# Kernel tuning notes

Hardware: AMD Instinct MI355X
Metric: run time of the kernel (lower is better)

The kernel has to match this reference:

```python
import jax, jax.numpy as jnp
import numpy as np

DIM = 180
HEADS = 6
WH, WW = 8, 8
MLP_HIDDEN = 720
EPS = 1e-5


def _rel_pos_index(wh, ww):
    ch = np.arange(wh)
    cw = np.arange(ww)
    coords = np.stack(np.meshgrid(ch, cw, indexing='ij'))  # [2, wh, ww]
    cf = coords.reshape(2, -1)                              # [2, N]
    rc = cf[:, :, None] - cf[:, None, :]                    # [2, N, N]
    rc = rc.transpose(1, 2, 0).astype(np.int64)             # [N, N, 2]
    rc[..., 0] += wh - 1
    rc[..., 1] += ww - 1
    rc[..., 0] *= 2 * ww - 1
    return rc.sum(-1)                                       # [N, N]


REL_IDX = jnp.asarray(_rel_pos_index(WH, WW))


def setup_inputs() -> dict:
    key = jax.random.key(0)
    ks = jax.random.split(key, 16)
    B, H, W = 8, 128, 128
    C = DIM
    s = lambda k, shape, sc=0.02: jax.random.normal(k, shape, jnp.float32) * sc
    return {
        'x': jax.random.normal(ks[0], (B, H * W, C), jnp.float32),
        'norm1_w': jnp.ones((C,), jnp.float32),
        'norm1_b': jnp.zeros((C,), jnp.float32),
        'qkv_w': s(ks[1], (C, 3 * C)),
        'qkv_b': jnp.zeros((3 * C,), jnp.float32),
        'rel_bias_table': s(ks[2], ((2 * WH - 1) * (2 * WW - 1), HEADS)),
        'proj_w': s(ks[3], (C, C)),
        'proj_b': jnp.zeros((C,), jnp.float32),
        'norm2_w': jnp.ones((C,), jnp.float32),
        'norm2_b': jnp.zeros((C,), jnp.float32),
        'fc1_w': s(ks[4], (C, MLP_HIDDEN)),
        'fc1_b': jnp.zeros((MLP_HIDDEN,), jnp.float32),
        'fc2_w': s(ks[5], (MLP_HIDDEN, C)),
        'fc2_b': jnp.zeros((C,), jnp.float32),
        'H': H,
        'W': W,
    }


def _layernorm(x, w, b):
    mu = jnp.mean(x, axis=-1, keepdims=True)
    var = jnp.var(x, axis=-1, keepdims=True)
    return (x - mu) * jax.lax.rsqrt(var + EPS) * w + b


def _swin_block(x, H, W, p):
    B, N, C = x.shape
    hd = C // HEADS
    scale = hd ** -0.5

    x1 = _layernorm(x, p['norm1_w'], p['norm1_b'])
    x1 = x1.reshape(B, H, W, C)
    # window partition -> [nW, WH*WW, C]
    x1 = x1.reshape(B, H // WH, WH, W // WW, WW, C).transpose(0, 1, 3, 2, 4, 5)
    nW = B * (H // WH) * (W // WW)
    Nw = WH * WW
    xw = x1.reshape(nW, Nw, C)

    qkv = xw @ p['qkv_w'] + p['qkv_b']                      # [nW, Nw, 3C]
    qkv = qkv.reshape(nW, Nw, 3, HEADS, hd).transpose(2, 0, 3, 1, 4)
    q, k, v = qkv[0], qkv[1], qkv[2]                        # [nW, H, Nw, hd]

    bias = p['rel_bias_table'][REL_IDX.reshape(-1)].reshape(Nw, Nw, HEADS)
    bias = bias.transpose(2, 0, 1)                          # [H, Nw, Nw]

    attn = jnp.einsum('whqd,whkd->whqk', q * scale, k) + bias[None]
    attn = jax.nn.softmax(attn, axis=-1)
    o = jnp.einsum('whqk,whkd->whqd', attn, v)              # [nW, H, Nw, hd]
    o = o.transpose(0, 2, 1, 3).reshape(nW, Nw, C)
    o = o @ p['proj_w'] + p['proj_b']

    # window reverse -> [B, H, W, C]
    o = o.reshape(B, H // WH, W // WW, WH, WW, C).transpose(0, 1, 3, 2, 4, 5)
    o = o.reshape(B, N, C)

    x1 = o + x
    x2 = _layernorm(x1, p['norm2_w'], p['norm2_b'])
    x2 = jax.nn.gelu(x2 @ p['fc1_w'] + p['fc1_b'], approximate=False) @ p['fc2_w'] + p['fc2_b']
    return x2 + x1


def reference(x, norm1_w, norm1_b, qkv_w, qkv_b, rel_bias_table, proj_w, proj_b,
              norm2_w, norm2_b, fc1_w, fc1_b, fc2_w, fc2_b, H, W):
    p = dict(norm1_w=norm1_w, norm1_b=norm1_b, qkv_w=qkv_w, qkv_b=qkv_b,
             rel_bias_table=rel_bias_table, proj_w=proj_w, proj_b=proj_b,
             norm2_w=norm2_w, norm2_b=norm2_b, fc1_w=fc1_w, fc1_b=fc1_b,
             fc2_w=fc2_w, fc2_b=fc2_b)
    return _swin_block(x, H, W, p)
```

## Files before the change

kernel.cpp:

```cpp
#include <hip/hip_runtime.h>
#include <hip/hip_bf16.h>

typedef __hip_bfloat16 bf16;
typedef __attribute__((ext_vector_type(8))) short short8;
typedef __attribute__((ext_vector_type(4))) short short4v;
typedef __attribute__((ext_vector_type(4))) float f32x4;

#define C_DIM 180
#define CPAD  192
#define NHEAD 6
#define HD    30
#define HID   720
#define HPAD  768
#define QKVW  576
#define LN_EPS 1e-5f
#define IMG_TOK 16384
#define QSCALE 0.18257418583505536f

static __device__ __forceinline__ bf16 f2bf(float f) { return __float2bfloat16(f); }
static __device__ __forceinline__ float bf2f(bf16 v) { return __bfloat162float(v); }
static __device__ __forceinline__ short bfbits(float f) {
    bf16 b = __float2bfloat16(f); return *reinterpret_cast<short*>(&b);
}
static __device__ __forceinline__ float gelu_tanh(float v) {
    float u = 0.7978845608f * (v + 0.044715f * v * v * v);
    float e = __expf(2.f * u);
    return 0.5f * v * (2.f - 2.f / (e + 1.f));
}

__global__ __launch_bounds__(256) void prep_w(const float* __restrict__ w, bf16* __restrict__ bt,
                                              int K, int N, int Kpad, int Npad) {
    int idx = blockIdx.x * 256 + threadIdx.x;
    if (idx >= Kpad * Npad) return;
    int k = idx % Kpad, n = idx / Kpad;
    float v = (k < K && n < N) ? w[(long)k * N + n] : 0.f;
    bt[idx] = f2bf(v);
}

__global__ __launch_bounds__(256) void prep_wqkv(const float* __restrict__ w, bf16* __restrict__ bt) {
    int idx = blockIdx.x * 256 + threadIdx.x;
    if (idx >= QKVW * CPAD) return;
    int k = idx % CPAD, c = idx / CPAD;
    int mat = c / 192, rem = c % 192;
    int hh = rem >> 5, dd = rem & 31;
    float v = 0.f;
    if (dd < HD && k < C_DIM) {
        v = w[(long)k * 540 + mat * 180 + hh * 30 + dd];
        if (mat == 0) v *= QSCALE;
    }
    bt[idx] = f2bf(v);
}
__global__ __launch_bounds__(256) void prep_bqkv(const float* __restrict__ b, float* __restrict__ bp) {
    int c = blockIdx.x * 256 + threadIdx.x;
    if (c >= QKVW) return;
    int mat = c / 192, rem = c % 192;
    int hh = rem >> 5, dd = rem & 31;
    float v = 0.f;
    if (dd < HD) {
        v = b[mat * 180 + hh * 30 + dd];
        if (mat == 0) v *= QSCALE;
    }
    bp[c] = v;
}

__global__ __launch_bounds__(256) void prep_f1b(const float* __restrict__ b, float* __restrict__ bp) {
    int i = blockIdx.x * 256 + threadIdx.x;
    if (i < HPAD) bp[i] = (i < HID) ? b[i] : 0.f;
}

__global__ __launch_bounds__(256) void prep_bias(const float* __restrict__ tbl,
                                                 float* __restrict__ bias_frag) {
    int idx = blockIdx.x * 256 + threadIdx.x;
    if (idx >= 6144) return;
    int lane = idx & 63;
    int fj = (idx >> 6) & 3;
    int fi = (idx >> 8) & 3;
    int h  = idx >> 10;
    int g = lane >> 4, l15 = lane & 15;
    int kk = fj * 16 + l15;
    int rk = kk >> 3, ck = kk & 7;
    #pragma unroll
    for (int r = 0; r < 4; ++r) {
        int q = fi * 16 + g * 4 + r;
        int rq = q >> 3, cq = q & 7;
        int bidx = (rq - rk + 7) * 15 + (cq - ck + 7);
        bias_frag[idx * 4 + r] = tbl[bidx * NHEAD + h];
    }
}

__global__ __launch_bounds__(256) void ln_kernel(const float* __restrict__ x,
                                                 const float* __restrict__ w,
                                                 const float* __restrict__ b,
                                                 bf16* __restrict__ out, int M) {
    int wave = threadIdx.x >> 6;
    int lane = threadIdx.x & 63;
    long row = (long)blockIdx.x * 4 + wave;
    if (row >= M) return;
    const float* xr = x + row * C_DIM;
    float e0 = xr[lane];
    float e1 = xr[lane + 64];
    float e2 = (lane < C_DIM - 128) ? xr[lane + 128] : 0.f;
    float s  = e0 + e1 + e2;
    float ss = e0*e0 + e1*e1 + e2*e2;
    #pragma unroll
    for (int off = 32; off > 0; off >>= 1) {
        s  += __shfl_xor(s,  off);
        ss += __shfl_xor(ss, off);
    }
    float mean = s * (1.f / C_DIM);
    float var  = ss * (1.f / C_DIM) - mean * mean;
    float rs   = rsqrtf(var + LN_EPS);
    bf16* orow = out + row * CPAD;
    orow[lane]      = f2bf((e0 - mean) * rs * w[lane]      + b[lane]);
    orow[lane + 64] = f2bf((e1 - mean) * rs * w[lane + 64] + b[lane + 64]);
    if (lane < C_DIM - 128)
        orow[lane + 128] = f2bf((e2 - mean) * rs * w[lane + 128] + b[lane + 128]);
    if (lane < CPAD - C_DIM)
        orow[C_DIM + lane] = f2bf(0.f);
}

#define GLL16(gp, lp) \
    __builtin_amdgcn_global_load_lds((const __attribute__((address_space(1))) unsigned int*)(gp), \
                                     (__attribute__((address_space(3))) unsigned int*)(lp), 16, 0, 0)

template<int DO_GELU, int OUT_MODE>
__global__ __launch_bounds__(256) void mfma_gemm(
    const bf16* __restrict__ A, int lda,
    const bf16* __restrict__ Bt,
    const float* __restrict__ bias,
    const float* __restrict__ resid, int nres,
    void* __restrict__ out, int ldo, int nstore,
    int Kpad, int P)
{
    __shared__ __align__(16) short smem[128 * 64 + 64 * 64];
    short* As = smem;
    short* Bs = smem + 128 * 64;
    int tid  = threadIdx.x;
    int lane = tid & 63;
    int wave = tid >> 6;
    int wm = wave >> 1, wn = wave & 1;
    int g4 = lane >> 4, l15 = lane & 15;

    int flat = blockIdx.x;
    int grp  = flat / (8 * P);
    int rem  = flat - grp * 8 * P;
    int p    = rem >> 3;
    long m0  = (long)(grp * 8 + (rem & 7)) * 128;
    int  n0  = p * 64;

    f32x4 acc[4][2] = {};

    int nkt = Kpad >> 6;
    for (int kt = 0; kt < nkt; ++kt) {
        int k0 = kt << 6;
        #pragma unroll
        for (int i = 0; i < 4; ++i) {
            int f = i * 256 + tid;
            int r = f >> 3, c = f & 7;
            const bf16* gp = A + (m0 + r) * (long)lda + k0 + ((c ^ (r & 7)) << 3);
            GLL16(gp, &As[(i * 256 + (wave << 6)) * 8]);
        }
        #pragma unroll
        for (int i = 0; i < 2; ++i) {
            int f = i * 256 + tid;
            int r = f >> 3, c = f & 7;
            const bf16* gp = Bt + (n0 + r) * (long)Kpad + k0 + ((c ^ (r & 7)) << 3);
            GLL16(gp, &Bs[(i * 256 + (wave << 6)) * 8]);
        }
        __syncthreads();
        #pragma unroll
        for (int ks = 0; ks < 2; ++ks) {
            short8 af[4], bfr[2];
            #pragma unroll
            for (int fi = 0; fi < 4; ++fi) {
                int r  = wm * 64 + fi * 16 + l15;
                int ch = ks * 4 + g4;
                af[fi] = *(const short8*)&As[r * 64 + ((ch ^ (r & 7)) << 3)];
            }
            #pragma unroll
            for (int fj = 0; fj < 2; ++fj) {
                int r  = wn * 32 + fj * 16 + l15;
                int ch = ks * 4 + g4;
                bfr[fj] = *(const short8*)&Bs[r * 64 + ((ch ^ (r & 7)) << 3)];
            }
            #pragma unroll
            for (int fi = 0; fi < 4; ++fi)
                #pragma unroll
                for (int fj = 0; fj < 2; ++fj)
                    acc[fi][fj] = __builtin_amdgcn_mfma_f32_16x16x32_bf16(af[fi], bfr[fj], acc[fi][fj], 0, 0, 0);
        }
        __syncthreads();
    }

    if (OUT_MODE == 0) {
        short* Cs = smem;
        #pragma unroll
        for (int fi = 0; fi < 4; ++fi)
            #pragma unroll
            for (int fj = 0; fj < 2; ++fj) {
                int col = wn * 32 + fj * 16 + l15;
                float bv = (n0 + col < nstore) ? bias[n0 + col] : 0.f;
                #pragma unroll
                for (int rg = 0; rg < 4; ++rg) {
                    int row = wm * 64 + fi * 16 + g4 * 4 + rg;
                    float v = acc[fi][fj][rg] + bv;
                    if (DO_GELU) v = gelu_tanh(v);
                    Cs[row * 72 + col] = bfbits(v);
                }
            }
        __syncthreads();
        #pragma unroll
        for (int i = 0; i < 4; ++i) {
            int t = i * 256 + tid;
            int row = t >> 3, c8 = t & 7;
            short8 v = *(const short8*)&Cs[row * 72 + c8 * 8];
            *(short8*)((bf16*)out + (m0 + row) * (long)ldo + n0 + c8 * 8) = v;
        }
    } else {
        float* Cf = (float*)smem;
        int ncols = nstore - n0; if (ncols > 64) ncols = 64;
        int cpr = ncols >> 2;
        #pragma unroll
        for (int hh = 0; hh < 2; ++hh) {
            if (wm == hh) {
                #pragma unroll
                for (int fi = 0; fi < 4; ++fi)
                    #pragma unroll
                    for (int fj = 0; fj < 2; ++fj) {
                        int col = wn * 32 + fj * 16 + l15;
                        float bv = (n0 + col < nstore) ? bias[n0 + col] : 0.f;
                        #pragma unroll
                        for (int rg = 0; rg < 4; ++rg) {
                            int lrow = fi * 16 + g4 * 4 + rg;
                            Cf[lrow * 68 + col] = acc[fi][fj][rg] + bv;
                        }
                    }
            }
            __syncthreads();
            for (int t = tid; t < 64 * cpr; t += 256) {
                int row = t / cpr, cc = (t - row * cpr) * 4;
                long grow = m0 + hh * 64 + row;
                f32x4 v = *(const f32x4*)&Cf[row * 68 + cc];
                if (resid) {
                    f32x4 rv = *(const f32x4*)(resid + grow * (long)nres + n0 + cc);
                    v += rv;
                }
                *(f32x4*)((float*)out + grow * (long)ldo + n0 + cc) = v;
            }
            __syncthreads();
        }
    }
}

__global__ __launch_bounds__(384, 3) void attn_mfma(
    const bf16* __restrict__ qkv,
    const float* __restrict__ bias_frag,
    bf16* __restrict__ o)
{
    __shared__ __align__(16) short lds[6 * 4096];
    int tid  = threadIdx.x;
    int wave = tid >> 6;
    int lane = tid & 63;
    int h = wave;
    int w = blockIdx.x;
    int b = w >> 8, rem = w & 255;
    int wi = rem >> 4, wj = rem & 15;
    long base = (long)b * IMG_TOK + wi * 8 * 128 + wj * 8;
    int g = lane >> 4, l15 = lane & 15;

    short* Vt = &lds[wave * 4096];
    short* Ph = &lds[wave * 4096 + 2048];

    short8 qf[4], kf[4];
    #pragma unroll
    for (int fi = 0; fi < 4; ++fi) {
        int q = fi * 16 + l15;
        long t = base + (q >> 3) * 128 + (q & 7);
        const bf16* rowp = qkv + t * QKVW + h * 32 + g * 8;
        qf[fi] = *(const short8*)(rowp);
        kf[fi] = *(const short8*)(rowp + 192);
    }

    {
        int t = lane;
        const bf16* vp = qkv + (base + (t >> 3) * 128 + (t & 7)) * QKVW + 384 + h * 32;
        short8 v0 = *(const short8*)(vp);
        short8 v1 = *(const short8*)(vp + 8);
        short8 v2 = *(const short8*)(vp + 16);
        short8 v3 = *(const short8*)(vp + 24);
        int ct = t >> 3, t7 = t & 7;
        #pragma unroll
        for (int d = 0; d < 8; ++d)  Vt[d * 64 + ((ct ^ d) << 3) + t7] = v0[d];
        #pragma unroll
        for (int d = 8; d < 16; ++d) Vt[d * 64 + ((ct ^ (d & 7)) << 3) + t7] = v1[d - 8];
        #pragma unroll
        for (int d = 16; d < 24; ++d) Vt[d * 64 + ((ct ^ (d & 7)) << 3) + t7] = v2[d - 16];
        #pragma unroll
        for (int d = 24; d < 32; ++d) Vt[d * 64 + ((ct ^ (d & 7)) << 3) + t7] = v3[d - 24];
    }

    f32x4 S[4][4];
    #pragma unroll
    for (int fi = 0; fi < 4; ++fi)
        #pragma unroll
        for (int fj = 0; fj < 4; ++fj)
            S[fi][fj] = *(const f32x4*)(bias_frag + (((h * 4 + fi) * 4 + fj) * 64 + lane) * 4);
    #pragma unroll
    for (int fi = 0; fi < 4; ++fi)
        #pragma unroll
        for (int fj = 0; fj < 4; ++fj)
            S[fi][fj] = __builtin_amdgcn_mfma_f32_16x16x32_bf16(qf[fi], kf[fj], S[fi][fj], 0, 0, 0);

    f32x4 mrow[4], lsum[4];
    #pragma unroll
    for (int fi = 0; fi < 4; ++fi) {
        f32x4 a = S[fi][0], c = S[fi][2];
        #pragma unroll
        for (int cc = 0; cc < 4; ++cc) {
            a[cc] = fmaxf(a[cc], S[fi][1][cc]);
            c[cc] = fmaxf(c[cc], S[fi][3][cc]);
            a[cc] = fmaxf(a[cc], c[cc]);
        }
        mrow[fi] = a;
    }
    #pragma unroll
    for (int mask = 1; mask <= 8; mask <<= 1)
        #pragma unroll
        for (int fi = 0; fi < 4; ++fi)
            #pragma unroll
            for (int cc = 0; cc < 4; ++cc)
                mrow[fi][cc] = fmaxf(mrow[fi][cc], __shfl_xor(mrow[fi][cc], mask));
    #pragma unroll
    for (int fi = 0; fi < 4; ++fi)
        #pragma unroll
        for (int fj = 0; fj < 4; ++fj)
            #pragma unroll
            for (int cc = 0; cc < 4; ++cc)
                S[fi][fj][cc] = __expf(S[fi][fj][cc] - mrow[fi][cc]);
    #pragma unroll
    for (int fi = 0; fi < 4; ++fi) {
        f32x4 a = S[fi][0] + S[fi][1];
        f32x4 c = S[fi][2] + S[fi][3];
        lsum[fi] = a + c;
    }
    #pragma unroll
    for (int mask = 1; mask <= 8; mask <<= 1)
        #pragma unroll
        for (int fi = 0; fi < 4; ++fi)
            #pragma unroll
            for (int cc = 0; cc < 4; ++cc)
                lsum[fi][cc] += __shfl_xor(lsum[fi][cc], mask);

    f32x4 O[4][2] = {};
    #pragma unroll
    for (int ks = 0; ks < 2; ++ks) {
        #pragma unroll
        for (int fi = 0; fi < 4; ++fi)
            #pragma unroll
            for (int f2 = 0; f2 < 2; ++f2) {
                int fj = ks * 2 + f2;
                int kh = f2 * 16 + l15;
                #pragma unroll
                for (int r = 0; r < 4; ++r) {
                    int q = fi * 16 + g * 4 + r;
                    int c = (kh >> 3) ^ r ^ g;
                    Ph[q * 32 + (c << 3) + (kh & 7)] = bfbits(S[fi][fj][r]);
                }
            }
        short8 vf[2];
        #pragma unroll
        for (int f2 = 0; f2 < 2; ++f2) {
            int d = f2 * 16 + l15;
            int cv = (ks * 4 + g) ^ (d & 7);
            vf[f2] = *(const short8*)&Vt[d * 64 + (cv << 3)];
        }
        #pragma unroll
        for (int fi = 0; fi < 4; ++fi) {
            int q = fi * 16 + l15;
            int cr = g ^ (q & 3) ^ ((q >> 2) & 3);
            short8 pf = *(const short8*)&Ph[q * 32 + (cr << 3)];
            #pragma unroll
            for (int f2 = 0; f2 < 2; ++f2)
                O[fi][f2] = __builtin_amdgcn_mfma_f32_16x16x32_bf16(pf, vf[f2], O[fi][f2], 0, 0, 0);
        }
    }

    #pragma unroll
    for (int fi = 0; fi < 4; ++fi) {
        f32x4 inv;
        #pragma unroll
        for (int cc = 0; cc < 4; ++cc) inv[cc] = 1.f / lsum[fi][cc];
        #pragma unroll
        for (int r = 0; r < 4; ++r) {
            int q = fi * 16 + g * 4 + r;
            long t = base + (q >> 3) * 128 + (q & 7);
            bf16* op = o + t * CPAD + h * HD;
            op[l15] = f2bf(O[fi][0][r] * inv[r]);
            if (l15 < HD - 16)
                op[16 + l15] = f2bf(O[fi][1][r] * inv[r]);
        }
    }
    if (h == 0) {
        long t = base + (lane >> 3) * 128 + (lane & 7);
        bf16* op = o + t * CPAD + C_DIM;
        short4v z4 = {0, 0, 0, 0};
        short8  z8 = {0, 0, 0, 0, 0, 0, 0, 0};
        *(short4v*)(op) = z4;
        *(short8*)(op + 4) = z8;
    }
}

extern "C" void kernel_launch(void* const* d_in, const int* in_sizes, int n_in,
                              void* d_out, int out_size, void* d_ws, size_t ws_size,
                              hipStream_t stream) {
    const float* x    = (const float*)d_in[0];
    const float* n1w  = (const float*)d_in[1];
    const float* n1b  = (const float*)d_in[2];
    const float* qkvw = (const float*)d_in[3];
    const float* qkvb = (const float*)d_in[4];
    const float* tbl  = (const float*)d_in[5];
    const float* pw   = (const float*)d_in[6];
    const float* pb   = (const float*)d_in[7];
    const float* n2w  = (const float*)d_in[8];
    const float* n2b  = (const float*)d_in[9];
    const float* f1w  = (const float*)d_in[10];
    const float* f1b  = (const float*)d_in[11];
    const float* f2w  = (const float*)d_in[12];
    const float* f2b  = (const float*)d_in[13];

    auto al = [](size_t b) { return (b + 255) & ~(size_t)255; };
    char* base = (char*)d_ws;
    size_t off = 0;
    auto alloc = [&](size_t bytes) -> char* { char* p = base + off; off += al(bytes); return p; };

    bf16* wqp  = (bf16*)alloc((size_t)QKVW * CPAD * 2);
    bf16* wp   = (bf16*)alloc((size_t)192 * 192 * 2);
    bf16* wf1  = (bf16*)alloc((size_t)768 * 192 * 2);
    bf16* wf2  = (bf16*)alloc((size_t)192 * 768 * 2);
    float* bfr = (float*)alloc((size_t)6144 * 4 * 4);
    float* f1bp = (float*)alloc((size_t)HPAD * 4);
    float* qbp  = (float*)alloc((size_t)QKVW * 4);
    size_t woff = off;

    size_t r1_per = al((size_t)IMG_TOK * HPAD * 2);
    size_t r2_per = al((size_t)IMG_TOK * CPAD * 2);
    size_t r3_per = al((size_t)IMG_TOK * C_DIM * 4);
    size_t per_img = r1_per + r2_per + r3_per;
    int g = 8;
    while (g > 1 && woff + per_img * (size_t)g > ws_size) g >>= 1;
    int nchunks = 8 / g;
    long Mc = (long)IMG_TOK * g;
    int nm = (int)(Mc / 128);

    bf16*  R1 = (bf16*)(base + woff);
    bf16*  R2 = (bf16*)(base + woff + r1_per * g);
    float* R3 = (float*)(base + woff + (r1_per + r2_per) * g);

    prep_wqkv<<<(QKVW * CPAD + 255) / 256, 256, 0, stream>>>(qkvw, wqp);
    prep_bqkv<<<(QKVW + 255) / 256, 256, 0, stream>>>(qkvb, qbp);
    prep_w<<<(192 * 192 + 255) / 256, 256, 0, stream>>>(pw, wp, 180, 180, 192, 192);
    prep_w<<<(768 * 192 + 255) / 256, 256, 0, stream>>>(f1w, wf1, 180, 720, 192, 768);
    prep_w<<<(192 * 768 + 255) / 256, 256, 0, stream>>>(f2w, wf2, 720, 180, 768, 192);
    prep_bias<<<(6144 + 255) / 256, 256, 0, stream>>>(tbl, bfr);
    prep_f1b<<<(HPAD + 255) / 256, 256, 0, stream>>>(f1b, f1bp);

    for (int ci = 0; ci < nchunks; ++ci) {
        const float* xc   = x + (size_t)ci * Mc * C_DIM;
        float*       outc = (float*)d_out + (size_t)ci * Mc * C_DIM;

        ln_kernel<<<Mc / 4, 256, 0, stream>>>(xc, n1w, n1b, R2, (int)Mc);
        mfma_gemm<0, 0><<<dim3(nm * 9), 256, 0, stream>>>(
            R2, CPAD, wqp, qbp, nullptr, 0, R1, QKVW, QKVW, CPAD, 9);
        attn_mfma<<<dim3(256 * g), 384, 0, stream>>>(R1, bfr, R2);
        mfma_gemm<0, 1><<<dim3(nm * 3), 256, 0, stream>>>(
            R2, CPAD, wp, pb, xc, 180, R3, 180, 180, CPAD, 3);
        ln_kernel<<<Mc / 4, 256, 0, stream>>>(R3, n2w, n2b, R2, (int)Mc);
        mfma_gemm<1, 0><<<dim3(nm * 12), 256, 0, stream>>>(
            R2, CPAD, wf1, f1bp, nullptr, 0, R1, HPAD, HPAD, CPAD, 12);
        mfma_gemm<0, 1><<<dim3(nm * 3), 256, 0, stream>>>(
            R1, HPAD, wf2, f2b, R3, 180, outc, 180, 180, HPAD, 3);
    }
}
```

Measured before the change: 483.7 us.

## Add 128x128-tile GEMM kernel for fc1 and use nontemporal stores

Introduces a new 512-thread MFMA GEMM with 128x128 output tiles and XOR-swizzled LDS, used for the fc1+GELU projection in place of the 128x64 tile kernel, halving the number of blocks and improving operand reuse per loaded tile. Also switches output stores in the existing GEMM epilogues to nontemporal stores to reduce cache pollution. The larger tile raises register and LDS use per block and may lower occupancy; nontemporal stores could hurt if the next kernel rereads the data from cache.

```diff
diff --git a/kernel.cpp b/kernel.cpp
--- a/kernel.cpp
+++ b/kernel.cpp
@@ -214,7 +214,7 @@
             int t = i * 256 + tid;
             int row = t >> 3, c8 = t & 7;
             short8 v = *(const short8*)&Cs[row * 72 + c8 * 8];
-            *(short8*)((bf16*)out + (m0 + row) * (long)ldo + n0 + c8 * 8) = v;
+            __builtin_nontemporal_store(v, (short8*)((bf16*)out + (m0 + row) * (long)ldo + n0 + c8 * 8));
         }
     } else {
         float* Cf = (float*)smem;
@@ -245,10 +245,104 @@
                     f32x4 rv = *(const f32x4*)(resid + grow * (long)nres + n0 + cc);
                     v += rv;
                 }
-                *(f32x4*)((float*)out + grow * (long)ldo + n0 + cc) = v;
+                __builtin_nontemporal_store(v, (f32x4*)((float*)out + grow * (long)ldo + n0 + cc));
             }
             __syncthreads();
         }
+    }
+}
+
+template<int DO_GELU>
+__global__ __launch_bounds__(512) void mfma_gemm128(
+    const bf16* __restrict__ A, int lda,
+    const bf16* __restrict__ Bt,
+    const float* __restrict__ bias,
+    bf16* __restrict__ out, int ldo,
+    int Kpad, int P)
+{
+    __shared__ __align__(16) short smem[128 * 64 + 128 * 64];
+    short* As = smem;
+    short* Bs = smem + 128 * 64;
+    int tid  = threadIdx.x;
+    int lane = tid & 63;
+    int wave = tid >> 6;
+    int wm = wave >> 1, wn = wave & 1;
+    int g4 = lane >> 4, l15 = lane & 15;
+
+    int flat = blockIdx.x;
+    int grp  = flat / (8 * P);
+    int rem  = flat - grp * 8 * P;
+    int p    = rem >> 3;
+    long m0  = (long)(grp * 8 + (rem & 7)) * 128;
+    int  n0  = p * 128;
+
+    f32x4 acc[2][4] = {};
+
+    int nkt = Kpad >> 6;
+    for (int kt = 0; kt < nkt; ++kt) {
+        int k0 = kt << 6;
+        #pragma unroll
+        for (int i = 0; i < 2; ++i) {
+            int f = i * 512 + tid;
+            int r = f >> 3, c = f & 7;
+            const bf16* gp = A + (m0 + r) * (long)lda + k0 + ((c ^ (r & 7)) << 3);
+            GLL16(gp, &As[(i * 512 + (wave << 6)) * 8]);
+        }
+        #pragma unroll
+        for (int i = 0; i < 2; ++i) {
+            int f = i * 512 + tid;
+            int r = f >> 3, c = f & 7;
+            const bf16* gp = Bt + (n0 + r) * (long)Kpad + k0 + ((c ^ (r & 7)) << 3);
+            GLL16(gp, &Bs[(i * 512 + (wave << 6)) * 8]);
+        }
+        __syncthreads();
+        #pragma unroll
+        for (int ks = 0; ks < 2; ++ks) {
+            short8 af[2], bfr[4];
+            #pragma unroll
+            for (int fi = 0; fi < 2; ++fi) {
+                int r  = wm * 32 + fi * 16 + l15;
+                int ch = ks * 4 + g4;
+                af[fi] = *(const short8*)&As[r * 64 + ((ch ^ (r & 7)) << 3)];
+            }
+            #pragma unroll
+            for (int fj = 0; fj < 4; ++fj) {
+                int r  = wn * 64 + fj * 16 + l15;
+                int ch = ks * 4 + g4;
+                bfr[fj] = *(const short8*)&Bs[r * 64 + ((ch ^ (r & 7)) << 3)];
+            }
+            #pragma unroll
+            for (int fi = 0; fi < 2; ++fi)
+                #pragma unroll
+                for (int fj = 0; fj < 4; ++fj)
+                    acc[fi][fj] = __builtin_amdgcn_mfma_f32_16x16x32_bf16(af[fi], bfr[fj], acc[fi][fj], 0, 0, 0);
+        }
+        __syncthreads();
+    }
+
+    short* Cs = smem;
+    #pragma unroll
+    for (int fi = 0; fi < 2; ++fi)
+        #pragma unroll
+        for (int fj = 0; fj < 4; ++fj) {
+            int col = wn * 64 + fj * 16 + l15;
+            float bv = bias[n0 + col];
+            #pragma unroll
+            for (int rg = 0; rg < 4; ++rg) {
+                int row = wm * 32 + fi * 16 + g4 * 4 + rg;
+                float v = acc[fi][fj][rg] + bv;
+                if (DO_GELU) v = gelu_tanh(v);
+                int ch = (col >> 3) ^ (row & 7);
+                Cs[row * 128 + (ch << 3) + (col & 7)] = bfbits(v);
+            }
+        }
+    __syncthreads();
+    #pragma unroll
+    for (int i = 0; i < 4; ++i) {
+        int t = i * 512 + tid;
+        int row = t >> 4, c16 = t & 15;
+        short8 v = *(const short8*)&Cs[row * 128 + ((c16 ^ (row & 7)) << 3)];
+        __builtin_nontemporal_store(v, (short8*)(out + (m0 + row) * (long)ldo + n0 + c16 * 8));
     }
 }
 
@@ -475,8 +569,8 @@
         mfma_gemm<0, 1><<<dim3(nm * 3), 256, 0, stream>>>(
             R2, CPAD, wp, pb, xc, 180, R3, 180, 180, CPAD, 3);
         ln_kernel<<<Mc / 4, 256, 0, stream>>>(R3, n2w, n2b, R2, (int)Mc);
-        mfma_gemm<1, 0><<<dim3(nm * 12), 256, 0, stream>>>(
-            R2, CPAD, wf1, f1bp, nullptr, 0, R1, HPAD, HPAD, CPAD, 12);
+        mfma_gemm128<1><<<dim3(nm * 6), 512, 0, stream>>>(
+            R2, CPAD, wf1, f1bp, R1, HPAD, CPAD, 6);
         mfma_gemm<0, 1><<<dim3(nm * 3), 256, 0, stream>>>(
             R1, HPAD, wf2, f2b, R3, 180, outc, 180, 180, HPAD, 3);
     }
```

Result: slower. 496.7 us (+2.7%).
